# Performance work log

Measured on AMD Instinct MI355X. Metric: run time of the kernel, lower is better.

The kernel has to match this reference:

```python
import jax, jax.numpy as jnp
import numpy as np

DIM = 256
QK_DIM = 256
NUM_HEADS = 8
N_WIN = 7
TOPK = 4
SCALE = QK_DIM ** (-0.5)


def setup_inputs() -> dict:
    key = jax.random.key(0)
    k1, k2, k3 = jax.random.split(key, 3)
    N, D, H, W, C = 2, 8, 56, 56, DIM
    x = jax.random.normal(k1, (N, D, H, W, C), dtype=jnp.float32)
    # QKVLinear: Linear(dim, qk_dim + qk_dim + dim)
    Wqkv = jax.random.normal(k2, (C, 2 * QK_DIM + DIM), dtype=jnp.float32) * 0.02
    bqkv = jnp.zeros((2 * QK_DIM + DIM,), dtype=jnp.float32)
    Wo = jax.random.normal(k3, (DIM, DIM), dtype=jnp.float32) * 0.02
    bo = jnp.zeros((DIM,), dtype=jnp.float32)
    return {"x": x, "Wqkv": Wqkv, "bqkv": bqkv, "Wo": Wo, "bo": bo}


def reference(x, Wqkv, bqkv, Wo, bo):
    N, D, H, W, C = x.shape
    j = i = N_WIN
    h, w = H // j, W // i
    p2, w2 = j * i, h * w
    n = N * D
    m = NUM_HEADS
    ch = QK_DIM // m   # qk head dim
    cv = DIM // m      # v head dim

    # n t (j h) (i w) c -> n t (j i) h w c
    xw = x.reshape(N, D, j, h, i, w, C).transpose(0, 1, 2, 4, 3, 5, 6)
    xw = xw.reshape(N, D, p2, h, w, C)

    # QKVLinear then split into q / kv
    qkv = xw @ Wqkv + bqkv                       # (N,D,p2,h,w,2qk+dim)
    q = qkv[..., :QK_DIM]                        # (N,D,p2,h,w,qk)
    kv = qkv[..., QK_DIM:]                       # (N,D,p2,h,w,qk+dim)

    # inter-frame shift: frame t uses kv of frame t+1; last frame keeps its own
    kv = jnp.concatenate([kv[:, 1:], kv[:, -1:]], axis=1)

    q = q.reshape(n, p2, h, w, QK_DIM)
    kv = kv.reshape(n, p2, h, w, QK_DIM + DIM)
    q_pix = q.reshape(n, p2, w2, QK_DIM)
    kv_pix = kv.reshape(n, p2, w2, QK_DIM + DIM)  # identity kv_down

    # window-level routing (diff_routing=False -> detached)
    q_win = jax.lax.stop_gradient(q.mean(axis=(2, 3)))                  # (n,p2,qk)
    k_win = jax.lax.stop_gradient(kv[..., :QK_DIM].mean(axis=(2, 3)))   # (n,p2,qk)
    attn_logit = jnp.einsum('npc,nqc->npq', q_win * SCALE, k_win)       # (n,p2,p2)
    topk_logit, r_idx = jax.lax.top_k(attn_logit, TOPK)                 # (n,p2,topk)
    r_weight = jax.nn.softmax(topk_logit, axis=-1)  # computed, unused (mul_weight='none')

    # gather kv of routed windows: (n,p2,topk,w2,qk+dim)
    kv_sel = jax.vmap(lambda kvp, idx: kvp[idx])(kv_pix, r_idx)

    k_sel = kv_sel[..., :QK_DIM].reshape(n, p2, TOPK * w2, m, ch)
    v_sel = kv_sel[..., QK_DIM:].reshape(n, p2, TOPK * w2, m, cv)
    qh = q_pix.reshape(n, p2, w2, m, ch)

    attn = jnp.einsum('npqmc,npkmc->npmqk', qh * SCALE, k_sel)  # (n,p2,m,w2,topk*w2)
    attn = jax.nn.softmax(attn, axis=-1)
    out = jnp.einsum('npmqk,npkmc->npqmc', attn, v_sel).reshape(n, p2, w2, C)

    # (n j i) (h w) c -> N D (j h) (i w) c
    out = out.reshape(N, D, j, i, h, w, C).transpose(0, 1, 2, 4, 3, 5, 6)
    out = out.reshape(N, D, H, W, C)
    out = out @ Wo + bo
    return out
```

## Files before the change

kernel.cpp:

```cpp
#include <hip/hip_runtime.h>
#include <hip/hip_bf16.h>
#include <math.h>

#define QSC 0.09016844f

typedef __attribute__((ext_vector_type(8))) short bf16x8;
typedef __attribute__((ext_vector_type(4))) float f32x4;

__device__ __forceinline__ ushort f2bf(float f) {
    unsigned u = __float_as_uint(f);
    return (ushort)((u + 0x7FFFu + ((u >> 16) & 1u)) >> 16);
}

__device__ __forceinline__ unsigned pk2bf(float a, float b) {
    __hip_bfloat162 h = __float22bfloat162_rn(make_float2(a, b));
    return *(unsigned*)&h;
}

__device__ __forceinline__ void gl_lds16(const ushort* g, ushort* l) {
    __builtin_amdgcn_global_load_lds(
        (const __attribute__((address_space(1))) unsigned int*)g,
        (__attribute__((address_space(3))) unsigned int*)l, 16, 0, 0);
}

__device__ __forceinline__ int swz(int row) { return (row ^ (row >> 2)) & 3; }

__global__ __launch_bounds__(256) void k_prep(const float* __restrict__ x,
                                              const float* __restrict__ Wqkv,
                                              const float* __restrict__ Wo,
                                              ushort* __restrict__ xg,
                                              float* __restrict__ xmean,
                                              ushort* __restrict__ Wqkvt,
                                              ushort* __restrict__ Wot) {
    int b = blockIdx.x;
    int tid = threadIdx.x;
    if (b >= 784) {
        int bb = b - 784;
        if (bb < 768) Wqkvt[bb * 256 + tid] = f2bf(Wqkv[(size_t)tid * 768 + bb]);
        else { int n = bb - 768; Wot[n * 256 + tid] = f2bf(Wo[(size_t)tid * 256 + n]); }
        return;
    }
    int nd = b / 49, p = b % 49;
    int j = p / 7, i = p % 7;
    const int cg = tid & 63;
    const int pg = tid >> 6;

    const float* xb = x + ((size_t)nd * 3136 + ((size_t)(j * 8 + pg * 2)) * 56 + i * 8) * 256 + cg * 4;
    ushort* xo = xg + (size_t)b * 64 * 256 + (size_t)pg * 16 * 256 + cg * 4;

    __shared__ float4 part[4][64];
    float4 s = make_float4(0.f, 0.f, 0.f, 0.f);
#pragma unroll
    for (int r = 0; r < 2; ++r)
#pragma unroll
        for (int w = 0; w < 8; ++w) {
            float4 v = *(const float4*)(xb + (size_t)(r * 56 + w) * 256);
            s.x += v.x; s.y += v.y; s.z += v.z; s.w += v.w;
            uint2 pk;
            pk.x = pk2bf(v.x, v.y);
            pk.y = pk2bf(v.z, v.w);
            *(uint2*)(xo + (size_t)(r * 8 + w) * 256) = pk;
        }
    part[pg][cg] = s;
    __syncthreads();
    if (tid < 64) {
        float4 a = part[0][tid], b4 = part[1][tid], c = part[2][tid], d = part[3][tid];
        float4 m;
        m.x = (a.x + b4.x + c.x + d.x) * (1.f / 64.f);
        m.y = (a.y + b4.y + c.y + d.y) * (1.f / 64.f);
        m.z = (a.z + b4.z + c.z + d.z) * (1.f / 64.f);
        m.w = (a.w + b4.w + c.w + d.w) * (1.f / 64.f);
        *(float4*)(xmean + (size_t)b * 256 + tid * 4) = m;
    }
}

__global__ __launch_bounds__(256) void k_winproj(const float* __restrict__ xmean,
                                                 const float* __restrict__ Wqkv,
                                                 const float* __restrict__ bqkv,
                                                 float* __restrict__ qwin,
                                                 float* __restrict__ kwin) {
    __shared__ float As[16 * 68];
    __shared__ float Bs[16 * 64];
    const int tid = threadIdx.x;
    const int m0 = blockIdx.y * 64;
    const int n0 = blockIdx.x * 64;

    const int ar = tid >> 2;
    const int ak = (tid & 3) * 4;
    const int arow = (m0 + ar < 784) ? (m0 + ar) : 783;
    const float* aptr = xmean + (size_t)arow * 256 + ak;

    const int bk = tid >> 4;
    const int bn = (tid & 15) * 4;
    const float* bptr = Wqkv + (size_t)bk * 768 + n0 + bn;

    const int ty = tid >> 4, tx = tid & 15;
    float acc[4][4] = {};

    for (int kt = 0; kt < 256; kt += 16) {
        float4 av = *(const float4*)(aptr + kt);
        float4 bv = *(const float4*)(bptr + (size_t)kt * 768);
        __syncthreads();
        As[(ak + 0) * 68 + ar] = av.x;
        As[(ak + 1) * 68 + ar] = av.y;
        As[(ak + 2) * 68 + ar] = av.z;
        As[(ak + 3) * 68 + ar] = av.w;
        *(float4*)&Bs[bk * 64 + bn] = bv;
        __syncthreads();
#pragma unroll
        for (int kk = 0; kk < 16; ++kk) {
            float4 a4 = *(const float4*)&As[kk * 68 + ty * 4];
            float4 b4 = *(const float4*)&Bs[kk * 64 + tx * 4];
            float a[4] = {a4.x, a4.y, a4.z, a4.w};
            float b[4] = {b4.x, b4.y, b4.z, b4.w};
#pragma unroll
            for (int ii = 0; ii < 4; ++ii)
#pragma unroll
                for (int jj = 0; jj < 4; ++jj) acc[ii][jj] += a[ii] * b[jj];
        }
    }
#pragma unroll
    for (int ii = 0; ii < 4; ++ii) {
        int t = m0 + ty * 4 + ii;
        if (t >= 784) continue;
#pragma unroll
        for (int jj = 0; jj < 4; ++jj) {
            int col = n0 + tx * 4 + jj;
            float v = acc[ii][jj] + bqkv[col];
            if (col < 256) qwin[(size_t)t * 256 + col] = v;
            else           kwin[(size_t)t * 256 + (col - 256)] = v;
        }
    }
}

__global__ __launch_bounds__(256) void k_route(const float* __restrict__ qwin,
                                               const float* __restrict__ kwin,
                                               int* __restrict__ ridx) {
    const int b = blockIdx.x;
    const int nd = b / 49;
    const int ndkv = ((nd & 7) == 7) ? nd : nd + 1;
    const int tid = threadIdx.x;
    const int t = tid & 63, w = tid >> 6;
    __shared__ float qs[256];
    __shared__ float part[4][64];
    qs[tid] = qwin[b * 256 + tid];
    __syncthreads();
    float s = 0.f;
    if (t < 49) {
        const float* kr = kwin + ((size_t)ndkv * 49 + t) * 256 + w * 64;
#pragma unroll
        for (int c = 0; c < 64; c += 4) {
            float4 k4 = *(const float4*)(kr + c);
            float4 q4 = *(const float4*)&qs[w * 64 + c];
            s += q4.x * k4.x + q4.y * k4.y + q4.z * k4.z + q4.w * k4.w;
        }
    }
    part[w][t] = s;
    __syncthreads();
    if (tid < 64) {
        float logit = (t < 49) ? (part[0][t] + part[1][t] + part[2][t] + part[3][t])
                               : -INFINITY;
        for (int sel = 0; sel < 4; ++sel) {
            float v = logit;
            int ix = t;
            for (int off = 32; off > 0; off >>= 1) {
                float ov = __shfl_xor(v, off);
                int   oi = __shfl_xor(ix, off);
                if (ov > v || (ov == v && oi < ix)) { v = ov; ix = oi; }
            }
            if (t == 0) ridx[b * 4 + sel] = ix;
            if (t == ix) logit = -INFINITY;
        }
    }
}

__global__ __launch_bounds__(256) void k_gemm_qkv(const ushort* __restrict__ A,
                                                  const ushort* __restrict__ Bt,
                                                  const float* __restrict__ bqkv,
                                                  ushort* __restrict__ q,
                                                  ushort* __restrict__ kv) {
    __shared__ ushort As[2][128 * 32];
    __shared__ ushort Bs[2][128 * 32];
    const int tid = threadIdx.x;
    const int wv = tid >> 6, ln = tid & 63;
    const int lane15 = ln & 15, quad = ln >> 4;

    const int lin  = blockIdx.x + blockIdx.y * 6;
    const int work = (lin & 7) * 294 + (lin >> 3);
    const int n0 = (work % 6) * 128;
    const int m0 = (work / 6) * 128;

    const int row0 = tid >> 2, ck0 = tid & 3;
    const ushort* gA[2]; const ushort* gB[2];
    int lofs[2];
#pragma unroll
    for (int p = 0; p < 2; ++p) {
        int r = p * 64 + row0;
        int cks = ck0 ^ swz(r);
        gA[p] = A  + (size_t)(m0 + r) * 256 + cks * 8;
        gB[p] = Bt + (size_t)(n0 + r) * 256 + cks * 8;
        lofs[p] = (p * 256 + tid) * 8;
    }

    f32x4 acc[4][4];
#pragma unroll
    for (int i = 0; i < 4; ++i)
#pragma unroll
        for (int j = 0; j < 4; ++j) acc[i][j] = (f32x4){0.f, 0.f, 0.f, 0.f};

    const int mb = (wv >> 1) * 64, nb = (wv & 1) * 64;

#pragma unroll
    for (int p = 0; p < 2; ++p) {
        gl_lds16(gA[p], &As[0][lofs[p]]);
        gl_lds16(gB[p], &Bs[0][lofs[p]]);
    }
    asm volatile("s_waitcnt vmcnt(0)" ::: "memory");
    __builtin_amdgcn_s_barrier();

    int cur = 0;
#pragma unroll
    for (int kt = 0; kt < 8; ++kt) {
        if (kt < 7) {
#pragma unroll
            for (int p = 0; p < 2; ++p) {
                gl_lds16(gA[p] + (kt + 1) * 32, &As[cur ^ 1][lofs[p]]);
                gl_lds16(gB[p] + (kt + 1) * 32, &Bs[cur ^ 1][lofs[p]]);
            }
        }
        __builtin_amdgcn_sched_barrier(0);
        bf16x8 aF[4], bF[4];
#pragma unroll
        for (int mt = 0; mt < 4; ++mt) {
            int r = mb + mt * 16 + lane15;
            aF[mt] = *(const bf16x8*)&As[cur][r * 32 + (quad ^ swz(r)) * 8];
        }
#pragma unroll
        for (int nt = 0; nt < 4; ++nt) {
            int r = nb + nt * 16 + lane15;
            bF[nt] = *(const bf16x8*)&Bs[cur][r * 32 + (quad ^ swz(r)) * 8];
        }
#pragma unroll
        for (int mt = 0; mt < 4; ++mt)
#pragma unroll
            for (int nt = 0; nt < 4; ++nt)
                acc[mt][nt] = __builtin_amdgcn_mfma_f32_16x16x32_bf16(aF[mt], bF[nt], acc[mt][nt], 0, 0, 0);
        __builtin_amdgcn_sched_barrier(0);
        asm volatile("s_waitcnt vmcnt(0)" ::: "memory");
        __builtin_amdgcn_s_barrier();
        cur ^= 1;
    }

#pragma unroll
    for (int mt = 0; mt < 4; ++mt) {
#pragma unroll
        for (int nt = 0; nt < 4; ++nt) {
            int col = n0 + nb + nt * 16 + lane15;
            float bias = bqkv[col];
#pragma unroll
            for (int r = 0; r < 4; ++r) {
                int t = m0 + mb + mt * 16 + quad * 4 + r;
                float v = acc[mt][nt][r] + bias;
                if (col < 256) q[(size_t)t * 256 + col] = f2bf(v * QSC);
                else           kv[(size_t)t * 512 + (col - 256)] = f2bf(v);
            }
        }
    }
}

__global__ __launch_bounds__(256) void k_gemm_o(const ushort* __restrict__ A,
                                                const ushort* __restrict__ Bt,
                                                const float* __restrict__ bo,
                                                float* __restrict__ out) {
    __shared__ ushort As[2][128 * 32];
    __shared__ ushort Bs[2][128 * 32];
    const int tid = threadIdx.x;
    const int wv = tid >> 6, ln = tid & 63;
    const int lane15 = ln & 15, quad = ln >> 4;

    const int lin  = blockIdx.x;
    const int work = (lin & 7) * 98 + (lin >> 3);
    const int n0 = (work % 2) * 128;
    const int m0 = (work / 2) * 128;

    const int row0 = tid >> 2, ck0 = tid & 3;
    const ushort* gA[2]; const ushort* gB[2];
    int lofs[2];
#pragma unroll
    for (int p = 0; p < 2; ++p) {
        int r = p * 64 + row0;
        int cks = ck0 ^ swz(r);
        gA[p] = A  + (size_t)(m0 + r) * 256 + cks * 8;
        gB[p] = Bt + (size_t)(n0 + r) * 256 + cks * 8;
        lofs[p] = (p * 256 + tid) * 8;
    }

    f32x4 acc[4][4];
#pragma unroll
    for (int i = 0; i < 4; ++i)
#pragma unroll
        for (int j = 0; j < 4; ++j) acc[i][j] = (f32x4){0.f, 0.f, 0.f, 0.f};

    const int mb = (wv >> 1) * 64, nb = (wv & 1) * 64;

#pragma unroll
    for (int p = 0; p < 2; ++p) {
        gl_lds16(gA[p], &As[0][lofs[p]]);
        gl_lds16(gB[p], &Bs[0][lofs[p]]);
    }
    asm volatile("s_waitcnt vmcnt(0)" ::: "memory");
    __builtin_amdgcn_s_barrier();

    int cur = 0;
#pragma unroll
    for (int kt = 0; kt < 8; ++kt) {
        if (kt < 7) {
#pragma unroll
            for (int p = 0; p < 2; ++p) {
                gl_lds16(gA[p] + (kt + 1) * 32, &As[cur ^ 1][lofs[p]]);
                gl_lds16(gB[p] + (kt + 1) * 32, &Bs[cur ^ 1][lofs[p]]);
            }
        }
        __builtin_amdgcn_sched_barrier(0);
        bf16x8 aF[4], bF[4];
#pragma unroll
        for (int mt = 0; mt < 4; ++mt) {
            int r = mb + mt * 16 + lane15;
            aF[mt] = *(const bf16x8*)&As[cur][r * 32 + (quad ^ swz(r)) * 8];
        }
#pragma unroll
        for (int nt = 0; nt < 4; ++nt) {
            int r = nb + nt * 16 + lane15;
            bF[nt] = *(const bf16x8*)&Bs[cur][r * 32 + (quad ^ swz(r)) * 8];
        }
#pragma unroll
        for (int mt = 0; mt < 4; ++mt)
#pragma unroll
            for (int nt = 0; nt < 4; ++nt)
                acc[mt][nt] = __builtin_amdgcn_mfma_f32_16x16x32_bf16(aF[mt], bF[nt], acc[mt][nt], 0, 0, 0);
        __builtin_amdgcn_sched_barrier(0);
        asm volatile("s_waitcnt vmcnt(0)" ::: "memory");
        __builtin_amdgcn_s_barrier();
        cur ^= 1;
    }

    const int w6 = (m0 + mb) >> 6;
    const int ndw = w6 / 49, pw = w6 % 49;
    const int wbase = ndw * 3136 + (pw / 7) * 8 * 56 + (pw % 7) * 8;
#pragma unroll
    for (int mt = 0; mt < 4; ++mt)
#pragma unroll
        for (int nt = 0; nt < 4; ++nt) {
            int col = n0 + nb + nt * 16 + lane15;
            float bias = bo[col];
#pragma unroll
            for (int r = 0; r < 4; ++r) {
                int pix = mt * 16 + quad * 4 + r;
                int xr = wbase + (pix >> 3) * 56 + (pix & 7);
                out[(size_t)xr * 256 + col] = acc[mt][nt][r] + bias;
            }
        }
}

__global__ __launch_bounds__(256, 4) void k_attn(ushort* qbuf,
                                                 const ushort* __restrict__ kvbuf,
                                                 const int* __restrict__ ridx) {
    const int lin  = blockIdx.x + (blockIdx.y + blockIdx.z * 49) * 8;
    const int work = (lin & 7) * 784 + (lin >> 3);
    const int h = work & 7;
    const int rest = work >> 3;
    const int p = rest % 49;
    const int nd = rest / 49;

    const int ndkv = ((nd & 7) == 7) ? nd : nd + 1;
    const int tid = threadIdx.x;
    const int wv = tid >> 6, ln = tid & 63;
    const int lane15 = ln & 15, quad = ln >> 4;

    __shared__ ushort Ks[256 * 32];
    __shared__ ushort Vt[32 * 264];
    ushort* Ps = Ks;

    const int rb = (nd * 49 + p) * 4;
    int wid[4];
#pragma unroll
    for (int i = 0; i < 4; ++i) wid[i] = ridx[rb + i];

    const size_t kvband = (size_t)ndkv * 49;

    {
        const int key_l = wv * 16 + (ln >> 2);
        const int ck = (ln ^ (ln >> 2) ^ (ln >> 4)) & 3;
#pragma unroll
        for (int i = 0; i < 4; ++i) {
            size_t trow = (kvband + wid[i]) * 64 + key_l;
            gl_lds16(kvbuf + trow * 512 + h * 32 + ck * 8,
                     &Ks[(i * 64 + wv * 16) * 32 + ln * 8]);
        }
    }

    const size_t qrow0 = (size_t)(nd * 49 + p) * 64;
    bf16x8 bQ = *(const bf16x8*)(qbuf + (qrow0 + wv * 16 + lane15) * 256 + h * 32 + quad * 8);

    {
        int key_l = (tid & 31) * 2;
        int ch0 = (tid >> 5) * 4;
#pragma unroll
        for (int i = 0; i < 4; ++i) {
            size_t trow = (kvband + wid[i]) * 64;
            const ushort* g0 = kvbuf + (trow + key_l) * 512 + 256 + h * 32 + ch0;
            const ushort* g1 = g0 + 512;
            ushort4 a = *(const ushort4*)g0;
            ushort4 b = *(const ushort4*)g1;
            int kg = i * 64 + key_l;
            *(unsigned*)&Vt[(ch0 + 0) * 264 + kg] = (unsigned)a.x | ((unsigned)b.x << 16);
            *(unsigned*)&Vt[(ch0 + 1) * 264 + kg] = (unsigned)a.y | ((unsigned)b.y << 16);
            *(unsigned*)&Vt[(ch0 + 2) * 264 + kg] = (unsigned)a.z | ((unsigned)b.z << 16);
            *(unsigned*)&Vt[(ch0 + 3) * 264 + kg] = (unsigned)a.w | ((unsigned)b.w << 16);
        }
    }

    __syncthreads();

    const int ksz = (lane15 ^ (lane15 >> 2)) & 3;
    f32x4 st[16];
    __builtin_amdgcn_s_setprio(1);
#pragma unroll
    for (int t = 0; t < 16; ++t) {
        bf16x8 aK = *(const bf16x8*)&Ks[(t * 16 + lane15) * 32 + (quad ^ ksz) * 8];
        st[t] = __builtin_amdgcn_mfma_f32_16x16x32_bf16(aK, bQ, (f32x4){0.f, 0.f, 0.f, 0.f}, 0, 0, 0);
    }
    __builtin_amdgcn_s_setprio(0);

    __syncthreads();

    float sum = 0.f;
#pragma unroll
    for (int t = 0; t < 16; ++t)
#pragma unroll
        for (int r = 0; r < 4; ++r) {
            float e = __builtin_amdgcn_exp2f(st[t][r]);
            st[t][r] = e;
            sum += e;
        }
    sum += __shfl_xor(sum, 16);
    sum += __shfl_xor(sum, 32);
    const float inv = 1.f / sum;

    f32x4 oacc[2] = {{0.f, 0.f, 0.f, 0.f}, {0.f, 0.f, 0.f, 0.f}};
    const int prow = (wv * 16 + lane15) * 72;
#pragma unroll
    for (int cc = 0; cc < 4; ++cc) {
#pragma unroll
        for (int tt = 0; tt < 4; ++tt) {
            int t = cc * 4 + tt;
            uint2 pk;
            pk.x = pk2bf(st[t][0], st[t][1]);
            pk.y = pk2bf(st[t][2], st[t][3]);
            *(uint2*)&Ps[prow + tt * 16 + quad * 4] = pk;
        }
        __builtin_amdgcn_s_setprio(1);
#pragma unroll
        for (int kt = 0; kt < 2; ++kt) {
            bf16x8 aP = *(const bf16x8*)&Ps[prow + kt * 32 + quad * 8];
#pragma unroll
            for (int nt = 0; nt < 2; ++nt) {
                bf16x8 bV = *(const bf16x8*)&Vt[(nt * 16 + lane15) * 264 + cc * 64 + kt * 32 + quad * 8];
                oacc[nt] = __builtin_amdgcn_mfma_f32_16x16x32_bf16(aP, bV, oacc[nt], 0, 0, 0);
            }
        }
        __builtin_amdgcn_s_setprio(0);
    }

#pragma unroll
    for (int nt = 0; nt < 2; ++nt)
#pragma unroll
        for (int r = 0; r < 4; ++r) {
            int row = wv * 16 + quad * 4 + r;
            qbuf[(qrow0 + row) * 256 + h * 32 + nt * 16 + lane15] = f2bf(oacc[nt][r] * inv);
        }
}

extern "C" void kernel_launch(void* const* d_in, const int* in_sizes, int n_in,
                              void* d_out, int out_size, void* d_ws, size_t ws_size,
                              hipStream_t stream) {
    const float* x    = (const float*)d_in[0];
    const float* Wqkv = (const float*)d_in[1];
    const float* bqkv = (const float*)d_in[2];
    const float* Wo   = (const float*)d_in[3];
    const float* bo   = (const float*)d_in[4];
    float* out = (float*)d_out;

    char* ws = (char*)d_ws;
    ushort* xg    = (ushort*)ws;                    ws += (size_t)50176 * 256 * 2;
    ushort* q     = (ushort*)ws;                    ws += (size_t)50176 * 256 * 2;
    ushort* kv    = (ushort*)ws;                    ws += (size_t)50176 * 512 * 2;
    ushort* Wqkvt = (ushort*)ws;                    ws += (size_t)768 * 256 * 2;
    ushort* Wot   = (ushort*)ws;                    ws += (size_t)256 * 256 * 2;
    float*  xmean = (float*)ws;                     ws += (size_t)784 * 256 * 4;
    float*  qwin  = (float*)ws;                     ws += (size_t)784 * 256 * 4;
    float*  kwin  = (float*)ws;                     ws += (size_t)784 * 256 * 4;
    int*    ridx  = (int*)ws;

    k_prep    <<<1808, 256, 0, stream>>>(x, Wqkv, Wo, xg, xmean, Wqkvt, Wot);
    k_winproj <<<dim3(8, 13), 256, 0, stream>>>(xmean, Wqkv, bqkv, qwin, kwin);
    k_route   <<<784, 256, 0, stream>>>(qwin, kwin, ridx);
    k_gemm_qkv<<<dim3(6, 392), 256, 0, stream>>>(xg, Wqkvt, bqkv, q, kv);
    k_attn    <<<dim3(8, 49, 16), 256, 0, stream>>>(q, kv, ridx);
    k_gemm_o  <<<784, 256, 0, stream>>>(q, Wot, bo, out);
}
```

Before: 226.4 us.

## Fuse window projection into QKV GEMM launch and skip unused kv frame writes

Merges the small window-mean projection GEMM into the large QKV GEMM launch as 104 extra blocks that branch off early, removing one kernel launch and its serialization. It also skips writing kv for frame 0 of each sequence, since the inter-frame shift means no query reads it. This relies on the attention kernel's kv indexing never touching those rows, and the extra blocks reuse the shared-memory buffers.

After: 225.7 us. Within noise of the previous version (-0.3%).

```diff
diff --git a/kernel.cpp b/kernel.cpp
--- a/kernel.cpp
+++ b/kernel.cpp
@@ -71,65 +71,6 @@
         m.z = (a.z + b4.z + c.z + d.z) * (1.f / 64.f);
         m.w = (a.w + b4.w + c.w + d.w) * (1.f / 64.f);
         *(float4*)(xmean + (size_t)b * 256 + tid * 4) = m;
-    }
-}
-
-__global__ __launch_bounds__(256) void k_winproj(const float* __restrict__ xmean,
-                                                 const float* __restrict__ Wqkv,
-                                                 const float* __restrict__ bqkv,
-                                                 float* __restrict__ qwin,
-                                                 float* __restrict__ kwin) {
-    __shared__ float As[16 * 68];
-    __shared__ float Bs[16 * 64];
-    const int tid = threadIdx.x;
-    const int m0 = blockIdx.y * 64;
-    const int n0 = blockIdx.x * 64;
-
-    const int ar = tid >> 2;
-    const int ak = (tid & 3) * 4;
-    const int arow = (m0 + ar < 784) ? (m0 + ar) : 783;
-    const float* aptr = xmean + (size_t)arow * 256 + ak;
-
-    const int bk = tid >> 4;
-    const int bn = (tid & 15) * 4;
-    const float* bptr = Wqkv + (size_t)bk * 768 + n0 + bn;
-
-    const int ty = tid >> 4, tx = tid & 15;
-    float acc[4][4] = {};
-
-    for (int kt = 0; kt < 256; kt += 16) {
-        float4 av = *(const float4*)(aptr + kt);
-        float4 bv = *(const float4*)(bptr + (size_t)kt * 768);
-        __syncthreads();
-        As[(ak + 0) * 68 + ar] = av.x;
-        As[(ak + 1) * 68 + ar] = av.y;
-        As[(ak + 2) * 68 + ar] = av.z;
-        As[(ak + 3) * 68 + ar] = av.w;
-        *(float4*)&Bs[bk * 64 + bn] = bv;
-        __syncthreads();
-#pragma unroll
-        for (int kk = 0; kk < 16; ++kk) {
-            float4 a4 = *(const float4*)&As[kk * 68 + ty * 4];
-            float4 b4 = *(const float4*)&Bs[kk * 64 + tx * 4];
-            float a[4] = {a4.x, a4.y, a4.z, a4.w};
-            float b[4] = {b4.x, b4.y, b4.z, b4.w};
-#pragma unroll
-            for (int ii = 0; ii < 4; ++ii)
-#pragma unroll
-                for (int jj = 0; jj < 4; ++jj) acc[ii][jj] += a[ii] * b[jj];
-        }
-    }
-#pragma unroll
-    for (int ii = 0; ii < 4; ++ii) {
-        int t = m0 + ty * 4 + ii;
-        if (t >= 784) continue;
-#pragma unroll
-        for (int jj = 0; jj < 4; ++jj) {
-            int col = n0 + tx * 4 + jj;
-            float v = acc[ii][jj] + bqkv[col];
-            if (col < 256) qwin[(size_t)t * 256 + col] = v;
-            else           kwin[(size_t)t * 256 + (col - 256)] = v;
-        }
     }
 }
 
@@ -174,18 +115,79 @@
     }
 }
 
-__global__ __launch_bounds__(256) void k_gemm_qkv(const ushort* __restrict__ A,
-                                                  const ushort* __restrict__ Bt,
-                                                  const float* __restrict__ bqkv,
-                                                  ushort* __restrict__ q,
-                                                  ushort* __restrict__ kv) {
+__global__ __launch_bounds__(256) void k_mega(const ushort* __restrict__ A,
+                                              const ushort* __restrict__ Bt,
+                                              const float* __restrict__ bqkv,
+                                              ushort* __restrict__ q,
+                                              ushort* __restrict__ kv,
+                                              const float* __restrict__ xmean,
+                                              const float* __restrict__ Wqkv,
+                                              float* __restrict__ qwin,
+                                              float* __restrict__ kwin) {
     __shared__ ushort As[2][128 * 32];
     __shared__ ushort Bs[2][128 * 32];
     const int tid = threadIdx.x;
+
+    if (blockIdx.x >= 2352) {
+        float* wAs = (float*)&As[0][0];
+        float* wBs = (float*)&Bs[0][0];
+        const int wb = blockIdx.x - 2352;
+        const int n0 = (wb & 7) * 64;
+        const int m0 = (wb >> 3) * 64;
+
+        const int ar = tid >> 2;
+        const int ak = (tid & 3) * 4;
+        const int arow = (m0 + ar < 784) ? (m0 + ar) : 783;
+        const float* aptr = xmean + (size_t)arow * 256 + ak;
+
+        const int bk = tid >> 4;
+        const int bn = (tid & 15) * 4;
+        const float* bptr = Wqkv + (size_t)bk * 768 + n0 + bn;
+
+        const int ty = tid >> 4, tx = tid & 15;
+        float acc[4][4] = {};
+
+        for (int kt = 0; kt < 256; kt += 16) {
+            float4 av = *(const float4*)(aptr + kt);
+            float4 bv = *(const float4*)(bptr + (size_t)kt * 768);
+            __syncthreads();
+            wAs[(ak + 0) * 68 + ar] = av.x;
+            wAs[(ak + 1) * 68 + ar] = av.y;
+            wAs[(ak + 2) * 68 + ar] = av.z;
+            wAs[(ak + 3) * 68 + ar] = av.w;
+            *(float4*)&wBs[bk * 64 + bn] = bv;
+            __syncthreads();
+#pragma unroll
+            for (int kk = 0; kk < 16; ++kk) {
+                float4 a4 = *(const float4*)&wAs[kk * 68 + ty * 4];
+                float4 b4 = *(const float4*)&wBs[kk * 64 + tx * 4];
+                float a[4] = {a4.x, a4.y, a4.z, a4.w};
+                float b[4] = {b4.x, b4.y, b4.z, b4.w};
+#pragma unroll
+                for (int ii = 0; ii < 4; ++ii)
+#pragma unroll
+                    for (int jj = 0; jj < 4; ++jj) acc[ii][jj] += a[ii] * b[jj];
+            }
+        }
+#pragma unroll
+        for (int ii = 0; ii < 4; ++ii) {
+            int t = m0 + ty * 4 + ii;
+            if (t >= 784) continue;
+#pragma unroll
+            for (int jj = 0; jj < 4; ++jj) {
+                int col = n0 + tx * 4 + jj;
+                float v = acc[ii][jj] + bqkv[col];
+                if (col < 256) qwin[(size_t)t * 256 + col] = v;
+                else           kwin[(size_t)t * 256 + (col - 256)] = v;
+            }
+        }
+        return;
+    }
+
     const int wv = tid >> 6, ln = tid & 63;
     const int lane15 = ln & 15, quad = ln >> 4;
 
-    const int lin  = blockIdx.x + blockIdx.y * 6;
+    const int lin  = blockIdx.x;
     const int work = (lin & 7) * 294 + (lin >> 3);
     const int n0 = (work % 6) * 128;
     const int m0 = (work / 6) * 128;
@@ -251,6 +253,9 @@
         cur ^= 1;
     }
 
+    const int ndblk = (m0 + mb) / 3136;
+    const bool wantkv = !(ndblk == 0 || ndblk == 8);
+
 #pragma unroll
     for (int mt = 0; mt < 4; ++mt) {
 #pragma unroll
@@ -262,7 +267,7 @@
                 int t = m0 + mb + mt * 16 + quad * 4 + r;
                 float v = acc[mt][nt][r] + bias;
                 if (col < 256) q[(size_t)t * 256 + col] = f2bf(v * QSC);
-                else           kv[(size_t)t * 512 + (col - 256)] = f2bf(v);
+                else if (wantkv) kv[(size_t)t * 512 + (col - 256)] = f2bf(v);
             }
         }
     }
@@ -502,10 +507,9 @@
     float*  kwin  = (float*)ws;                     ws += (size_t)784 * 256 * 4;
     int*    ridx  = (int*)ws;
 
-    k_prep    <<<1808, 256, 0, stream>>>(x, Wqkv, Wo, xg, xmean, Wqkvt, Wot);
-    k_winproj <<<dim3(8, 13), 256, 0, stream>>>(xmean, Wqkv, bqkv, qwin, kwin);
-    k_route   <<<784, 256, 0, stream>>>(qwin, kwin, ridx);
-    k_gemm_qkv<<<dim3(6, 392), 256, 0, stream>>>(xg, Wqkvt, bqkv, q, kv);
-    k_attn    <<<dim3(8, 49, 16), 256, 0, stream>>>(q, kv, ridx);
-    k_gemm_o  <<<784, 256, 0, stream>>>(q, Wot, bo, out);
-}
+    k_prep  <<<1808, 256, 0, stream>>>(x, Wqkv, Wo, xg, xmean, Wqkvt, Wot);
+    k_mega  <<<2456, 256, 0, stream>>>(xg, Wqkvt, bqkv, q, kv, xmean, Wqkv, qwin, kwin);
+    k_route <<<784, 256, 0, stream>>>(qwin, kwin, ridx);
+    k_attn  <<<dim3(8, 49, 16), 256, 0, stream>>>(q, kv, ridx);
+    k_gemm_o<<<784, 256, 0, stream>>>(q, Wot, bo, out);
+}
```
